# Optimization experiments

Measured on AMD Instinct MI355X. Metric: run time of the kernel, lower is better.

The kernel has to match this reference:

```python
import jax, jax.numpy as jnp
import numpy as np

SIZE = 128
RATIO = 0.5

def setup_inputs() -> dict:
    key = jax.random.key(0)
    k1, k2, k3 = jax.random.split(key, 3)
    B, D, K = 16, 256, 18
    assp_features = jax.random.normal(k1, (B, D, SIZE, SIZE), dtype=jnp.float32)
    prototypes = jax.random.normal(k2, (B, K, D), dtype=jnp.float32)
    n_samp = int(SIZE * SIZE * RATIO)
    # sample without replacement, matching np.random.choice(replace=False)
    random_indices = jax.random.permutation(k3, SIZE * SIZE)[:n_samp].astype(jnp.int64)
    return {"assp_features": assp_features, "prototypes": prototypes,
            "random_indices": random_indices}

def reference(assp_features, prototypes, random_indices):
    # assp_features: [B, D, H, W], prototypes: [B, K, D], random_indices: [N]
    size = assp_features.shape[-1]
    x = random_indices // size  # [N]
    y = random_indices % size   # [N]
    f = assp_features[:, :, x, y]            # [B, D, N] gathered pixel features
    # squared L2 distances [B, N, K]; argmin of ||p-f||_2 == argmin of squared dist
    p2 = jnp.sum(prototypes * prototypes, axis=-1)       # [B, K]
    f2 = jnp.sum(f * f, axis=1)                          # [B, N]
    cross = jnp.einsum('bdn,bkd->bnk', f, prototypes)    # [B, N, K]
    d2 = p2[:, None, :] - 2.0 * cross + f2[:, :, None]
    idx = jnp.argmin(d2, axis=-1)                        # [B, N]
    nearest = jnp.take_along_axis(prototypes, idx[..., None], axis=1)  # [B, N, D]
    out = assp_features.at[:, :, x, y].set(jnp.swapaxes(nearest, 1, 2))
    return out
```

## Files before the change

### kernel.cpp

```cpp
#include <hip/hip_runtime.h>

constexpr int B = 16;
constexpr int D = 256;
constexpr int K = 18;
constexpr int SZ = 128;
constexpr int S = SZ * SZ;
constexpr int N = S / 2;
constexpr int PB = 64;

__global__ __launch_bounds__(256) void prep_kernel(
    const float* __restrict__ proto,
    const int* __restrict__ idx,
    unsigned char* __restrict__ mask,
    double* __restrict__ p2,
    double* __restrict__ p64) {
  const int blk = blockIdx.x;
  if (blk < 32) {
    mask[idx[blk * 256 + threadIdx.x]] = 1;
  } else if (blk < 104) {
    const int row  = (blk - 32) * 4 + (threadIdx.x >> 6);
    const int lane = threadIdx.x & 63;
    const float4 v = *(const float4*)(proto + (size_t)row * D + lane * 4);
    double s = (double)v.x * (double)v.x + (double)v.y * (double)v.y
             + (double)v.z * (double)v.z + (double)v.w * (double)v.w;
#pragma unroll
    for (int off = 1; off < 64; off <<= 1)
      s += __shfl_xor(s, off, 64);
    if (lane == 0) p2[row] = s;
  } else {
    const int e = (blk - 104) * 256 + threadIdx.x;
    const int b = e / (D * K);
    const int r = e - b * (D * K);
    const int d = r / K;
    const int k = r - d * K;
    p64[e] = (double)proto[((size_t)b * K + k) * D + d];
  }
}

__global__ __launch_bounds__(256) void fused_kernel(
    const float* __restrict__ assp,
    const float* __restrict__ proto,
    const double* __restrict__ p64,
    const double* __restrict__ p2,
    const unsigned char* __restrict__ mask,
    float* __restrict__ out) {
  __shared__ float  fs[D][PB];
  __shared__ double red[4][6][PB];

  const int b     = blockIdx.x & 15;
  const int chunk = blockIdx.x >> 4;
  const int pos0  = chunk * PB;
  const int w     = __builtin_amdgcn_readfirstlane(threadIdx.x >> 6);
  const int lane  = threadIdx.x & 63;

  const float* fin = assp + (size_t)(b * D) * S + pos0;
  {
    const int dr = threadIdx.x >> 4;
    const int p4 = threadIdx.x & 15;
    for (int i = 0; i < 16; i += 4) {
      float4 v[4];
#pragma unroll
      for (int j = 0; j < 4; ++j)
        v[j] = *(const float4*)(fin + (size_t)((i + j) * 16 + dr) * S + p4 * 4);
#pragma unroll
      for (int j = 0; j < 4; ++j)
        *(float4*)&fs[(i + j) * 16 + dr][p4 * 4] = v[j];
    }
  }
  __syncthreads();

  double acc[K];
#pragma unroll
  for (int k = 0; k < K; ++k) acc[k] = 0.0;
  const double* pw = p64 + ((size_t)b * D + w * 64) * K;
  for (int i = 0; i < 64; ++i) {
    const double f = (double)fs[w * 64 + i][lane];
    const double* pr = pw + i * K;
#pragma unroll
    for (int k = 0; k < K; ++k) acc[k] += f * pr[k];
  }

  const double* p2b = p2 + b * K;
  double best = 1e300;
  int kstar = 0;
  for (int c = 0; c < 3; ++c) {
    __syncthreads();
#pragma unroll
    for (int j = 0; j < 6; ++j) red[w][j][lane] = acc[c * 6 + j];
    __syncthreads();
#pragma unroll
    for (int j = 0; j < 6; ++j) {
      const double s = ((red[0][j][lane] + red[1][j][lane]) + red[2][j][lane])
                     + red[3][j][lane];
      const double d2 = p2b[c * 6 + j] - 2.0 * s;
      if (d2 < best) { best = d2; kstar = c * 6 + j; }
    }
  }

  const int m = mask[pos0 + lane];
  float* op = out + ((size_t)(b * D + w * 64)) * S + pos0;
  const float* pkf = proto + ((size_t)(b * K + kstar)) * D + w * 64;
  for (int i = 0; i < 64; i += 4) {
    const float4 pv = *(const float4*)(pkf + i);
    const float f0 = fs[w * 64 + i + 0][lane];
    const float f1 = fs[w * 64 + i + 1][lane];
    const float f2 = fs[w * 64 + i + 2][lane];
    const float f3 = fs[w * 64 + i + 3][lane];
    op[(size_t)(i + 0) * S + lane] = m ? pv.x : f0;
    op[(size_t)(i + 1) * S + lane] = m ? pv.y : f1;
    op[(size_t)(i + 2) * S + lane] = m ? pv.z : f2;
    op[(size_t)(i + 3) * S + lane] = m ? pv.w : f3;
  }
}

extern "C" void kernel_launch(void* const* d_in, const int* in_sizes, int n_in,
                              void* d_out, int out_size, void* d_ws, size_t ws_size,
                              hipStream_t stream) {
  const float* assp  = (const float*)d_in[0];
  const float* proto = (const float*)d_in[1];
  const int*   idx   = (const int*)d_in[2];
  float* out = (float*)d_out;

  unsigned char* mask = (unsigned char*)d_ws;
  double*        p2   = (double*)((char*)d_ws + S);
  double*        p64  = (double*)((char*)d_ws + S + (size_t)B * K * 8);

  hipMemsetAsync(mask, 0, S, stream);
  prep_kernel<<<392, 256, 0, stream>>>(proto, idx, mask, p2, p64);
  fused_kernel<<<B * (S / PB), 256, 0, stream>>>(assp, proto, p64, p2, mask, out);
}
```

Before: 212.5 us.

## Restructure fused kernel: per-thread pixels with full-D accumulation, prototypes in LDS

Each thread now owns four pixels and accumulates all 18 distances over the full 256 channels in registers, instead of splitting D across waves and reducing through shared memory. The per-batch fp64 prototype matrix is staged in LDS, and blocks cover 512 pixels with 128 threads. Features are reread from global memory in the write-back pass rather than kept in LDS, and a transposed fp32 prototype copy serves the output gather. This removes the cross-wave reduction and its barriers, at the cost of a 72-register fp64 accumulator (pressure and occupancy risk), a second read of the input, and only 512 blocks.

```diff
diff --git a/kernel.cpp b/kernel.cpp
--- a/kernel.cpp
+++ b/kernel.cpp
@@ -6,14 +6,15 @@
 constexpr int SZ = 128;
 constexpr int S = SZ * SZ;
 constexpr int N = S / 2;
-constexpr int PB = 64;
+constexpr int PB = 512;
 
 __global__ __launch_bounds__(256) void prep_kernel(
     const float* __restrict__ proto,
     const int* __restrict__ idx,
     unsigned char* __restrict__ mask,
     double* __restrict__ p2,
-    double* __restrict__ p64) {
+    double* __restrict__ p64,
+    float* __restrict__ pT32) {
   const int blk = blockIdx.x;
   if (blk < 32) {
     mask[idx[blk * 256 + threadIdx.x]] = 1;
@@ -33,83 +34,98 @@
     const int r = e - b * (D * K);
     const int d = r / K;
     const int k = r - d * K;
-    p64[e] = (double)proto[((size_t)b * K + k) * D + d];
+    const float v = proto[((size_t)b * K + k) * D + d];
+    p64[e]  = (double)v;
+    pT32[e] = v;
   }
 }
 
-__global__ __launch_bounds__(256) void fused_kernel(
+__global__ __launch_bounds__(128, 2) void fused_kernel(
     const float* __restrict__ assp,
-    const float* __restrict__ proto,
     const double* __restrict__ p64,
+    const float* __restrict__ pT32,
     const double* __restrict__ p2,
     const unsigned char* __restrict__ mask,
     float* __restrict__ out) {
-  __shared__ float  fs[D][PB];
-  __shared__ double red[4][6][PB];
+  __shared__ double spd[D * K];
 
   const int b     = blockIdx.x & 15;
   const int chunk = blockIdx.x >> 4;
   const int pos0  = chunk * PB;
-  const int w     = __builtin_amdgcn_readfirstlane(threadIdx.x >> 6);
-  const int lane  = threadIdx.x & 63;
+  const int tid   = threadIdx.x;
 
-  const float* fin = assp + (size_t)(b * D) * S + pos0;
-  {
-    const int dr = threadIdx.x >> 4;
-    const int p4 = threadIdx.x & 15;
-    for (int i = 0; i < 16; i += 4) {
-      float4 v[4];
-#pragma unroll
-      for (int j = 0; j < 4; ++j)
-        v[j] = *(const float4*)(fin + (size_t)((i + j) * 16 + dr) * S + p4 * 4);
-#pragma unroll
-      for (int j = 0; j < 4; ++j)
-        *(float4*)&fs[(i + j) * 16 + dr][p4 * 4] = v[j];
-    }
-  }
+  const double* pb = p64 + (size_t)b * D * K;
+  for (int i = tid; i < D * K; i += 128) spd[i] = pb[i];
   __syncthreads();
 
-  double acc[K];
+  const float* fin = assp + (size_t)(b * D) * S + pos0 + 2 * tid;
+
+  double acc[4][K];
 #pragma unroll
-  for (int k = 0; k < K; ++k) acc[k] = 0.0;
-  const double* pw = p64 + ((size_t)b * D + w * 64) * K;
-  for (int i = 0; i < 64; ++i) {
-    const double f = (double)fs[w * 64 + i][lane];
-    const double* pr = pw + i * K;
+  for (int jp = 0; jp < 4; ++jp)
 #pragma unroll
-    for (int k = 0; k < K; ++k) acc[k] += f * pr[k];
+    for (int k = 0; k < K; ++k) acc[jp][k] = 0.0;
+
+  for (int d0 = 0; d0 < D; d0 += 8) {
+    float2 fv[8][2];
+#pragma unroll
+    for (int jd = 0; jd < 8; ++jd) {
+      fv[jd][0] = *(const float2*)(fin + (size_t)(d0 + jd) * S);
+      fv[jd][1] = *(const float2*)(fin + (size_t)(d0 + jd) * S + 256);
+    }
+#pragma unroll
+    for (int jd = 0; jd < 8; ++jd) {
+      const double f0 = (double)fv[jd][0].x;
+      const double f1 = (double)fv[jd][0].y;
+      const double f2 = (double)fv[jd][1].x;
+      const double f3 = (double)fv[jd][1].y;
+      const double* pr = &spd[(d0 + jd) * K];
+#pragma unroll
+      for (int k = 0; k < K; ++k) {
+        const double pk = pr[k];
+        acc[0][k] += f0 * pk;
+        acc[1][k] += f1 * pk;
+        acc[2][k] += f2 * pk;
+        acc[3][k] += f3 * pk;
+      }
+    }
   }
 
   const double* p2b = p2 + b * K;
-  double best = 1e300;
-  int kstar = 0;
-  for (int c = 0; c < 3; ++c) {
-    __syncthreads();
+  double best[4];
+  int kst[4];
 #pragma unroll
-    for (int j = 0; j < 6; ++j) red[w][j][lane] = acc[c * 6 + j];
-    __syncthreads();
+  for (int jp = 0; jp < 4; ++jp) { best[jp] = 1e300; kst[jp] = 0; }
 #pragma unroll
-    for (int j = 0; j < 6; ++j) {
-      const double s = ((red[0][j][lane] + red[1][j][lane]) + red[2][j][lane])
-                     + red[3][j][lane];
-      const double d2 = p2b[c * 6 + j] - 2.0 * s;
-      if (d2 < best) { best = d2; kstar = c * 6 + j; }
+  for (int k = 0; k < K; ++k) {
+    const double pk2 = p2b[k];
+#pragma unroll
+    for (int jp = 0; jp < 4; ++jp) {
+      const double d2 = pk2 - 2.0 * acc[jp][k];
+      if (d2 < best[jp]) { best[jp] = d2; kst[jp] = k; }
     }
   }
 
-  const int m = mask[pos0 + lane];
-  float* op = out + ((size_t)(b * D + w * 64)) * S + pos0;
-  const float* pkf = proto + ((size_t)(b * K + kstar)) * D + w * 64;
-  for (int i = 0; i < 64; i += 4) {
-    const float4 pv = *(const float4*)(pkf + i);
-    const float f0 = fs[w * 64 + i + 0][lane];
-    const float f1 = fs[w * 64 + i + 1][lane];
-    const float f2 = fs[w * 64 + i + 2][lane];
-    const float f3 = fs[w * 64 + i + 3][lane];
-    op[(size_t)(i + 0) * S + lane] = m ? pv.x : f0;
-    op[(size_t)(i + 1) * S + lane] = m ? pv.y : f1;
-    op[(size_t)(i + 2) * S + lane] = m ? pv.z : f2;
-    op[(size_t)(i + 3) * S + lane] = m ? pv.w : f3;
+  const uchar2 m0 = *(const uchar2*)(mask + pos0 + 2 * tid);
+  const uchar2 m1 = *(const uchar2*)(mask + pos0 + 256 + 2 * tid);
+  const float* pt = pT32 + (size_t)b * D * K;
+  float* op = out + (size_t)(b * D) * S + pos0 + 2 * tid;
+
+  for (int d0 = 0; d0 < D; d0 += 8) {
+#pragma unroll
+    for (int jd = 0; jd < 8; ++jd) {
+      const int d = d0 + jd;
+      const float2 fa = *(const float2*)(fin + (size_t)d * S);
+      const float2 fb = *(const float2*)(fin + (size_t)d * S + 256);
+      const float* prow = pt + d * K;
+      float2 oa, ob;
+      oa.x = m0.x ? prow[kst[0]] : fa.x;
+      oa.y = m0.y ? prow[kst[1]] : fa.y;
+      ob.x = m1.x ? prow[kst[2]] : fb.x;
+      ob.y = m1.y ? prow[kst[3]] : fb.y;
+      *(float2*)(op + (size_t)d * S) = oa;
+      *(float2*)(op + (size_t)d * S + 256) = ob;
+    }
   }
 }
 
@@ -124,8 +140,9 @@
   unsigned char* mask = (unsigned char*)d_ws;
   double*        p2   = (double*)((char*)d_ws + S);
   double*        p64  = (double*)((char*)d_ws + S + (size_t)B * K * 8);
+  float*         pT32 = (float*)((char*)p64 + (size_t)B * D * K * 8);
 
   hipMemsetAsync(mask, 0, S, stream);
-  prep_kernel<<<392, 256, 0, stream>>>(proto, idx, mask, p2, p64);
-  fused_kernel<<<B * (S / PB), 256, 0, stream>>>(assp, proto, p64, p2, mask, out);
+  prep_kernel<<<392, 256, 0, stream>>>(proto, idx, mask, p2, p64, pT32);
+  fused_kernel<<<B * (S / PB), 128, 0, stream>>>(assp, p64, pT32, p2, mask, out);
 }
```

New measurement: 229.9 us. 1.08x slower.
